# Kernel tuning notes

Hardware: AMD Instinct MI355X
Metric: run time of the kernel (lower is better)

## Reference

```python
import jax, jax.numpy as jnp
import numpy as np

NEG_MASK = -10000.0

def setup_inputs() -> dict:
    key = jax.random.key(0)
    k1, k2 = jax.random.split(key)
    T, H, E = 16384, 4096, 64
    hidden_states = jax.random.normal(k1, (T, H), dtype=jnp.float32)
    # router weight [E, H], scaled like typical init so logits are O(1)
    weight = jax.random.normal(k2, (E, H), dtype=jnp.float32) / np.sqrt(H)
    allowed_ids = jnp.arange(32, dtype=jnp.int64 if jax.config.jax_enable_x64 else jnp.int32)
    return {"hidden_states": hidden_states, "weight": weight, "allowed_ids": allowed_ids}

def reference(hidden_states, weight, allowed_ids):
    TOP_K = 8
    E = weight.shape[0]
    # router logits: [T, E]
    router_logits = jnp.einsum("th,eh->te", hidden_states, weight)
    # training-time mask: experts not in allowed_ids get -10000 (allowed_ids are unique,
    # so the scatter of gathered values equals a boolean where-select)
    allowed_mask = jnp.zeros((E,), dtype=bool).at[allowed_ids].set(True)
    router_logits = jnp.where(allowed_mask[None, :], router_logits, NEG_MASK)
    # softmax over experts in float32
    routing_weights = jax.nn.softmax(router_logits.astype(jnp.float32), axis=1)
    # top-k + renorm
    routing_weights, selected_experts = jax.lax.top_k(routing_weights, TOP_K)
    routing_weights = routing_weights / jnp.sum(routing_weights, axis=-1, keepdims=True)
    return (router_logits, routing_weights.astype(hidden_states.dtype), selected_experts)
```

## Files before the change

kernel.cpp:

```cpp
#include <hip/hip_runtime.h>
#include <hip/hip_bf16.h>

typedef __attribute__((ext_vector_type(16))) float f32x16;
typedef __attribute__((ext_vector_type(8))) short short8v;
typedef __attribute__((ext_vector_type(8))) unsigned short ushort8v;

#define T_ROWS 16384
#define H_DIM  4096
#define E_NUM  64
#define TOPK   8
#define MROWS  64
#define KC     128
#define NCH    (H_DIM / KC)
#define WIMG   16384
#define MASK_OFF ((size_t)NCH * WIMG)

__device__ __forceinline__ unsigned short f2bf(float f) {
    unsigned int u = __float_as_uint(f);
    unsigned int r = (u + 0x7fffu + ((u >> 16) & 1u)) >> 16;
    return (unsigned short)r;
}
__device__ __forceinline__ float bf2f(unsigned short h) {
    return __uint_as_float(((unsigned int)h) << 16);
}
__device__ __forceinline__ void gload_lds16(const void* g, void* l) {
    __builtin_amdgcn_global_load_lds(
        (const __attribute__((address_space(1))) unsigned int*)g,
        (__attribute__((address_space(3))) unsigned int*)l, 16, 0, 0);
}

__global__ __launch_bounds__(256) void prep_w(
    const float* __restrict__ W, unsigned short* __restrict__ WS,
    const int* __restrict__ ids, int nids)
{
    const int g     = blockIdx.x * 256 + threadIdx.x;
    const int byteo = g * 16;
    const int ch    = byteo >> 14;
    const int rem   = byteo & 16383;
    const int row   = rem >> 8;
    const int sb    = rem & 255;
    const int bc    = sb ^ ((row & 15) << 4);
    const float* src = W + (size_t)row * H_DIM + ch * KC + (bc >> 1);
    ushort8v o;
#pragma unroll
    for (int t = 0; t < 8; ++t) o[t] = f2bf(src[t]);
    *(ushort8v*)((char*)WS + byteo) = o;

    if (blockIdx.x == 0 && threadIdx.x == 0) {
        unsigned long long mb = 0;
        for (int t = 0; t < nids; ++t) {
            const int e = ids[t];
            if (e >= 0 && e < E_NUM) mb |= (1ull << e);
        }
        *(unsigned long long*)((char*)WS + MASK_OFF) = mb;
    }
}

__global__ __launch_bounds__(1024) void router_main(
    const float* __restrict__ X, const unsigned short* __restrict__ WS,
    float* __restrict__ out)
{
    const int tid  = threadIdx.x;
    const int lane = tid & 63;
    const int w    = tid >> 6;
    const int kh   = w & 3;
    const int cg   = (w >> 2) & 1;
    const int rg   = w >> 3;
    const int rb   = blockIdx.x * MROWS;
    const int fr32 = lane & 31;
    const int fo   = lane >> 5;

    __shared__ char LDSRAW[65536];
    char* XH  = LDSRAW;
    char* XL  = LDSRAW + 16384;
    char* WT0 = LDSRAW + 32768;
    char* WT1 = LDSRAW + 49152;

    const int srow  = tid >> 4;
    const int sc8   = (tid & 15) * 8;
    const float* xg = X + (size_t)(rb + srow) * H_DIM + sc8;
    const int xbyte = srow * 256 + ((sc8 * 2) ^ ((srow & 15) << 4));

    const char* wimg = (const char*)WS;
    const int   woff = w * 1024 + lane * 16;

    const int arow = rg * 32 + fr32;
    const int asw  = (arow & 15) << 4;
    const int brow = cg * 32 + fr32;
    const int bsw  = (brow & 15) << 4;

    f32x16 acc;
#pragma unroll
    for (int r = 0; r < 16; ++r) acc[r] = 0.f;

    float4 px0 = *(const float4*)(xg);
    float4 px1 = *(const float4*)(xg + 4);
    gload_lds16(wimg + woff, WT0 + woff);

    for (int ch = 0; ch < NCH; ++ch) {
        __syncthreads();
        {
            float v[8] = {px0.x, px0.y, px0.z, px0.w,
                          px1.x, px1.y, px1.z, px1.w};
            ushort8v hv, lv;
#pragma unroll
            for (int t = 0; t < 8; ++t) {
                const unsigned short hb = f2bf(v[t]);
                hv[t] = hb;
                lv[t] = f2bf(v[t] - bf2f(hb));
            }
            *(ushort8v*)(XH + xbyte) = hv;
            *(ushort8v*)(XL + xbyte) = lv;
        }
        __syncthreads();
        if (ch + 1 < NCH) {
            const float* xn = xg + (ch + 1) * KC;
            px0 = *(const float4*)(xn);
            px1 = *(const float4*)(xn + 4);
            gload_lds16(wimg + (size_t)(ch + 1) * WIMG + woff,
                        ((ch & 1) ? WT0 : WT1) + woff);
        }
        const char* wt = (ch & 1) ? WT1 : WT0;
#pragma unroll
        for (int ks = 0; ks < 2; ++ks) {
            const int kb = kh * 64 + ks * 32 + fo * 16;
            short8v ah = *(const short8v*)(XH + arow * 256 + (kb ^ asw));
            short8v al = *(const short8v*)(XL + arow * 256 + (kb ^ asw));
            short8v bh = *(const short8v*)(wt + brow * 256 + (kb ^ bsw));
            acc = __builtin_amdgcn_mfma_f32_32x32x16_bf16(ah, bh, acc, 0, 0, 0);
            acc = __builtin_amdgcn_mfma_f32_32x32x16_bf16(al, bh, acc, 0, 0, 0);
        }
    }

    __syncthreads();
    float* sm = (float*)LDSRAW;
    if (kh < 2) {
#pragma unroll
        for (int r = 0; r < 16; ++r) {
            const int row = (r & 3) + 8 * (r >> 2) + 4 * fo;
            sm[(kh * 64 + rg * 32 + row) * 68 + cg * 32 + fr32] = acc[r];
        }
    }
    __syncthreads();
    if (kh >= 2) {
#pragma unroll
        for (int r = 0; r < 16; ++r) {
            const int row = (r & 3) + 8 * (r >> 2) + 4 * fo;
            sm[((kh - 2) * 64 + rg * 32 + row) * 68 + cg * 32 + fr32] += acc[r];
        }
    }
    __syncthreads();
    if (w >= 4) return;

    const unsigned long long mbits =
        *(const unsigned long long*)((const char*)WS + MASK_OFF);

    const int fr = lane & 15;
    const int fq = lane >> 4;
    float* o_log = out;
    float* o_rw  = out + (size_t)T_ROWS * E_NUM;
    float* o_se  = o_rw + (size_t)T_ROWS * TOPK;

#pragma unroll
    for (int j = 0; j < 4; ++j) {
        const int row_l = w * 16 + fq * 4 + j;
        const int grow  = rb + row_l;
        float a0 = 0.f, a1 = 0.f, a2 = 0.f, a3 = 0.f;
#pragma unroll
        for (int p = 0; p < 2; ++p) {
            a0 += sm[(p * 64 + row_l) * 68 +  0 + fr];
            a1 += sm[(p * 64 + row_l) * 68 + 16 + fr];
            a2 += sm[(p * 64 + row_l) * 68 + 32 + fr];
            a3 += sm[(p * 64 + row_l) * 68 + 48 + fr];
        }
        float mv0 = ((mbits >> ( 0 + fr)) & 1) ? a0 : -10000.0f;
        float mv1 = ((mbits >> (16 + fr)) & 1) ? a1 : -10000.0f;
        float mv2 = ((mbits >> (32 + fr)) & 1) ? a2 : -10000.0f;
        float mv3 = ((mbits >> (48 + fr)) & 1) ? a3 : -10000.0f;
        o_log[(size_t)grow * 64 +  0 + fr] = mv0;
        o_log[(size_t)grow * 64 + 16 + fr] = mv1;
        o_log[(size_t)grow * 64 + 32 + fr] = mv2;
        o_log[(size_t)grow * 64 + 48 + fr] = mv3;

        float m = fmaxf(fmaxf(mv0, mv1), fmaxf(mv2, mv3));
#pragma unroll
        for (int off = 1; off < 16; off <<= 1) m = fmaxf(m, __shfl_xor(m, off));

        float tsum = 0.f, myv = 0.f;
        int   mye  = 0;
#pragma unroll
        for (int t = 0; t < TOPK; ++t) {
            float bv = mv0; int be = fr;
            if (mv1 > bv) { bv = mv1; be = 16 + fr; }
            if (mv2 > bv) { bv = mv2; be = 32 + fr; }
            if (mv3 > bv) { bv = mv3; be = 48 + fr; }
#pragma unroll
            for (int off = 1; off < 16; off <<= 1) {
                float ov = __shfl_xor(bv, off);
                int   oe = __shfl_xor(be, off);
                if (ov > bv || (ov == bv && oe < be)) { bv = ov; be = oe; }
            }
            const float pv = expf(bv - m);
            tsum += pv;
            if (fr == t) { myv = pv; mye = be; }
            if ((be & 15) == fr) {
                const int bn = be >> 4;
                if      (bn == 0) mv0 = -3.4e38f;
                else if (bn == 1) mv1 = -3.4e38f;
                else if (bn == 2) mv2 = -3.4e38f;
                else              mv3 = -3.4e38f;
            }
        }
        if (fr < TOPK) {
            o_rw[(size_t)grow * TOPK + fr] = myv / tsum;
            o_se[(size_t)grow * TOPK + fr] = (float)mye;
        }
    }
}

extern "C" void kernel_launch(void* const* d_in, const int* in_sizes, int n_in,
                              void* d_out, int out_size, void* d_ws, size_t ws_size,
                              hipStream_t stream) {
    const float* X   = (const float*)d_in[0];
    const float* W   = (const float*)d_in[1];
    const int*   ids = (const int*)d_in[2];
    const int    nids = in_sizes[2];
    float* out = (float*)d_out;

    unsigned short* WS = (unsigned short*)d_ws;

    hipLaunchKernelGGL(prep_w, dim3(128), dim3(256), 0, stream, W, WS, ids, nids);
    hipLaunchKernelGGL(router_main, dim3(T_ROWS / MROWS), dim3(1024), 0, stream,
                       X, WS, out);
}
```

Baseline: 77.86 us.

## Double-buffer converted X tiles in LDS and prefetch two chunks ahead

X is now held in two LDS buffers, each with hi and lo bf16 halves, and total LDS grows to 96KB. Each iteration converts and stores the next chunk into the idle buffer while MFMAs read the current one. This removes one of the two per-chunk __syncthreads, and the global loads of X now run two chunks ahead to hide more memory latency. The cost is higher LDS use per block, which may lower how many blocks fit on a CU, and more registers live across each iteration.

Result: no change. 76.55 us (-1.7%).

```diff
diff --git a/kernel.cpp b/kernel.cpp
--- a/kernel.cpp
+++ b/kernel.cpp
@@ -70,11 +70,7 @@
     const int fr32 = lane & 31;
     const int fo   = lane >> 5;
 
-    __shared__ char LDSRAW[65536];
-    char* XH  = LDSRAW;
-    char* XL  = LDSRAW + 16384;
-    char* WT0 = LDSRAW + 32768;
-    char* WT1 = LDSRAW + 49152;
+    __shared__ char LDSRAW[98304];
 
     const int srow  = tid >> 4;
     const int sc8   = (tid & 15) * 8;
@@ -95,13 +91,27 @@
 
     float4 px0 = *(const float4*)(xg);
     float4 px1 = *(const float4*)(xg + 4);
-    gload_lds16(wimg + woff, WT0 + woff);
+    gload_lds16(wimg + woff, LDSRAW + 65536 + woff);
+    {
+        float v[8] = {px0.x, px0.y, px0.z, px0.w, px1.x, px1.y, px1.z, px1.w};
+        ushort8v hv, lv;
+#pragma unroll
+        for (int t = 0; t < 8; ++t) {
+            const unsigned short hb = f2bf(v[t]);
+            hv[t] = hb;
+            lv[t] = f2bf(v[t] - bf2f(hb));
+        }
+        *(ushort8v*)(LDSRAW + xbyte)         = hv;
+        *(ushort8v*)(LDSRAW + 16384 + xbyte) = lv;
+    }
+    px0 = *(const float4*)(xg + KC);
+    px1 = *(const float4*)(xg + KC + 4);
 
     for (int ch = 0; ch < NCH; ++ch) {
+        const int p = ch & 1;
         __syncthreads();
-        {
-            float v[8] = {px0.x, px0.y, px0.z, px0.w,
-                          px1.x, px1.y, px1.z, px1.w};
+        if (ch + 1 < NCH) {
+            float v[8] = {px0.x, px0.y, px0.z, px0.w, px1.x, px1.y, px1.z, px1.w};
             ushort8v hv, lv;
 #pragma unroll
             for (int t = 0; t < 8; ++t) {
@@ -109,23 +119,25 @@
                 hv[t] = hb;
                 lv[t] = f2bf(v[t] - bf2f(hb));
             }
-            *(ushort8v*)(XH + xbyte) = hv;
-            *(ushort8v*)(XL + xbyte) = lv;
-        }
-        __syncthreads();
-        if (ch + 1 < NCH) {
-            const float* xn = xg + (ch + 1) * KC;
+            char* xb = LDSRAW + (p ^ 1) * 32768;
+            *(ushort8v*)(xb + xbyte)         = hv;
+            *(ushort8v*)(xb + 16384 + xbyte) = lv;
+            gload_lds16(wimg + (size_t)(ch + 1) * WIMG + woff,
+                        LDSRAW + 65536 + (p ^ 1) * 16384 + woff);
+        }
+        if (ch + 2 < NCH) {
+            const float* xn = xg + (ch + 2) * KC;
             px0 = *(const float4*)(xn);
             px1 = *(const float4*)(xn + 4);
-            gload_lds16(wimg + (size_t)(ch + 1) * WIMG + woff,
-                        ((ch & 1) ? WT0 : WT1) + woff);
-        }
-        const char* wt = (ch & 1) ? WT1 : WT0;
+        }
+        const char* xh = LDSRAW + p * 32768;
+        const char* xl = xh + 16384;
+        const char* wt = LDSRAW + 65536 + p * 16384;
 #pragma unroll
         for (int ks = 0; ks < 2; ++ks) {
             const int kb = kh * 64 + ks * 32 + fo * 16;
-            short8v ah = *(const short8v*)(XH + arow * 256 + (kb ^ asw));
-            short8v al = *(const short8v*)(XL + arow * 256 + (kb ^ asw));
+            short8v ah = *(const short8v*)(xh + arow * 256 + (kb ^ asw));
+            short8v al = *(const short8v*)(xl + arow * 256 + (kb ^ asw));
             short8v bh = *(const short8v*)(wt + brow * 256 + (kb ^ bsw));
             acc = __builtin_amdgcn_mfma_f32_32x32x16_bf16(ah, bh, acc, 0, 0, 0);
             acc = __builtin_amdgcn_mfma_f32_32x32x16_bf16(al, bh, acc, 0, 0, 0);
```
